# Kernel optimization log

Hardware: AMD Instinct MI355X
Metric: run time of the kernel (lower is better)

## Reference

```python
import jax, jax.numpy as jnp
import numpy as np

N_QUBITS = 8
C64 = jnp.complex64

# ---- gate matrices ----

def u3(t, p, l):
    c = jnp.cos(t / 2).astype(C64)
    s = jnp.sin(t / 2).astype(C64)
    ep = jnp.exp(1j * p).astype(C64)
    el = jnp.exp(1j * l).astype(C64)
    return jnp.stack([jnp.stack([c, -el * s]),
                      jnp.stack([ep * s, ep * el * c])])

def ry(t):
    c = jnp.cos(t / 2).astype(C64)
    s = jnp.sin(t / 2).astype(C64)
    return jnp.stack([jnp.stack([c, -s]), jnp.stack([s, c])])

def rz(t):
    e = jnp.exp(-0.5j * t).astype(C64)
    z = jnp.zeros((), C64)
    return jnp.stack([jnp.stack([e, z]), jnp.stack([z, jnp.conj(e)])])

CNOT = jnp.array([[1, 0, 0, 0], [0, 1, 0, 0], [0, 0, 0, 1], [0, 0, 1, 0]], C64)
PX = jnp.array([[0, 1], [1, 0]], C64)
PY = jnp.array([[0, -1j], [1j, 0]], C64)
PZ = jnp.array([[1, 0], [0, -1]], C64)

# ---- batched state-vector gate application; psi: [B] + [2]*8, wire 0 = axis 1 (MSB) ----

def apply_1q(psi, U, w):
    psi = jnp.moveaxis(psi, w + 1, -1)
    psi = psi @ U.T
    return jnp.moveaxis(psi, -1, w + 1)

def apply_2q(psi, U4, w0, w1):
    psi = jnp.moveaxis(psi, (w0 + 1, w1 + 1), (-2, -1))
    sh = psi.shape
    psi = (psi.reshape(sh[:-2] + (4,)) @ U4.T).reshape(sh)
    return jnp.moveaxis(psi, (-2, -1), (w0 + 1, w1 + 1))

def u_su4(psi, p, w0, w1):
    psi = apply_1q(psi, u3(p[0], p[1], p[2]), w0)
    psi = apply_1q(psi, u3(p[3], p[4], p[5]), w1)
    psi = apply_2q(psi, CNOT, w0, w1)
    psi = apply_1q(psi, ry(p[6]), w0)
    psi = apply_1q(psi, rz(p[7]), w1)
    psi = apply_2q(psi, CNOT, w1, w0)
    psi = apply_1q(psi, ry(p[8]), w0)
    psi = apply_2q(psi, CNOT, w0, w1)
    psi = apply_1q(psi, u3(p[9], p[10], p[11]), w0)
    psi = apply_1q(psi, u3(p[12], p[13], p[14]), w1)
    return psi

LAYER1 = [(0, 1), (2, 3), (4, 5), (6, 7), (1, 2), (3, 4), (5, 6), (7, 0)]
LAYER2 = [(2, 4), (6, 0), (0, 2), (4, 6)]
LAYER3 = [(2, 6)]

def expval(psi, ops):
    phi = psi
    for M, w in ops:
        phi = apply_1q(phi, M, w)
    return jnp.real(jnp.sum(jnp.conj(psi) * phi, axis=tuple(range(1, N_QUBITS + 1))))

def circuit(x, weights):
    # amplitude embedding with normalization
    psi = (x / jnp.linalg.norm(x, axis=1, keepdims=True)).astype(C64)
    psi = psi.reshape((x.shape[0],) + (2,) * N_QUBITS)
    npc = 15
    layers = [LAYER1, LAYER1, LAYER2, LAYER2, LAYER3]
    for i, wires in enumerate(layers):
        p = weights[i * npc:(i + 1) * npc]
        for (w0, w1) in wires:
            psi = u_su4(psi, p, w0, w1)
    meas = [
        expval(psi, [(PX, 2)]), expval(psi, [(PY, 2)]), expval(psi, [(PZ, 2)]),
        expval(psi, [(PX, 6)]), expval(psi, [(PY, 6)]), expval(psi, [(PZ, 6)]),
        expval(psi, [(PX, 2), (PX, 6)]),
        expval(psi, [(PY, 2), (PY, 6)]),
        expval(psi, [(PZ, 2), (PZ, 6)]),
    ]
    return jnp.stack(meas, axis=1)  # [B, 9]


def setup_inputs() -> dict:
    key = jax.random.key(0)
    k1, k2 = jax.random.split(key)
    x = jax.random.normal(k1, (8192, 256), dtype=jnp.float32)
    weights = jax.random.normal(k2, (75,), dtype=jnp.float32)
    return {"x": x, "weights": weights}


def reference(x, weights):
    return circuit(x, weights)
```

## Files before the change

### kernel.cpp

```cpp
#include <hip/hip_runtime.h>

typedef float f32x2 __attribute__((ext_vector_type(2)));
typedef f32x2 c32;

__device__ __forceinline__ c32 mkc(float x, float y) { c32 r; r[0] = x; r[1] = y; return r; }

__device__ __forceinline__ c32 cmul(c32 a, c32 b) {
    c32 r;
    asm("v_pk_mul_f32 %0, %1, %2 op_sel:[0,0] op_sel_hi:[0,1]\n\t"
        "v_pk_fma_f32 %0, %1, %2, %0 op_sel:[1,1,0] op_sel_hi:[1,0,1] neg_lo:[1,0,0]"
        : "=&v"(r) : "v"(a), "v"(b));
    return r;
}
__device__ __forceinline__ c32 cmad(c32 a, c32 b, c32 acc) {
    asm("v_pk_fma_f32 %0, %1, %2, %0 op_sel:[0,0,0] op_sel_hi:[0,1,1]\n\t"
        "v_pk_fma_f32 %0, %1, %2, %0 op_sel:[1,1,0] op_sel_hi:[1,0,1] neg_lo:[1,0,0]"
        : "+v"(acc) : "v"(a), "v"(b));
    return acc;
}


__device__ __forceinline__ void mk_u3(float th, float ph, float la, c32 U[2][2]) {
    float ct = cosf(0.5f * th), st = sinf(0.5f * th);
    U[0][0] = mkc(ct, 0.f);
    U[0][1] = mkc(-cosf(la) * st, -sinf(la) * st);
    U[1][0] = mkc(cosf(ph) * st, sinf(ph) * st);
    U[1][1] = mkc(cosf(ph + la) * ct, sinf(ph + la) * ct);
}

__device__ __forceinline__ void lmul_kron(const c32 A[2][2], const c32 B[2][2], c32 m[4]) {
    c32 t[4];
#pragma unroll
    for (int r = 0; r < 4; ++r) {
        c32 acc = mkc(0.f, 0.f);
#pragma unroll
        for (int k = 0; k < 4; ++k)
            acc = cmad(cmul(A[r >> 1][k >> 1], B[r & 1][k & 1]), m[k], acc);
        t[r] = acc;
    }
#pragma unroll
    for (int r = 0; r < 4; ++r) m[r] = t[r];
}

__device__ void build_col(const float* __restrict__ w, int t, c32* gml) {
    const int g = t >> 2, c = t & 3;
    const float* p = w + g * 15;
    const int c0 = c >> 1, c1 = c & 1;
    c32 A[2][2], B[2][2], m[4], tmp;

    mk_u3(p[0], p[1], p[2], A);
    mk_u3(p[3], p[4], p[5], B);
#pragma unroll
    for (int r = 0; r < 4; ++r) m[r] = cmul(A[r >> 1][c0], B[r & 1][c1]);
    tmp = m[2]; m[2] = m[3]; m[3] = tmp;
    {
        float cc = cosf(0.5f * p[6]), s = sinf(0.5f * p[6]);
        A[0][0] = mkc(cc, 0.f); A[0][1] = mkc(-s, 0.f);
        A[1][0] = mkc(s, 0.f);  A[1][1] = mkc(cc, 0.f);
        float cz = cosf(0.5f * p[7]), sz = sinf(0.5f * p[7]);
        B[0][0] = mkc(cz, -sz); B[0][1] = mkc(0.f, 0.f);
        B[1][0] = mkc(0.f, 0.f); B[1][1] = mkc(cz, sz);
        lmul_kron(A, B, m);
    }
    tmp = m[1]; m[1] = m[3]; m[3] = tmp;
    {
        float cc = cosf(0.5f * p[8]), s = sinf(0.5f * p[8]);
        A[0][0] = mkc(cc, 0.f); A[0][1] = mkc(-s, 0.f);
        A[1][0] = mkc(s, 0.f);  A[1][1] = mkc(cc, 0.f);
        B[0][0] = mkc(1.f, 0.f); B[0][1] = mkc(0.f, 0.f);
        B[1][0] = mkc(0.f, 0.f); B[1][1] = mkc(1.f, 0.f);
        lmul_kron(A, B, m);
    }
    tmp = m[2]; m[2] = m[3]; m[3] = tmp;
    mk_u3(p[9], p[10], p[11], A);
    mk_u3(p[12], p[13], p[14], B);
    lmul_kron(A, B, m);
#pragma unroll
    for (int r = 0; r < 4; ++r) gml[g * 16 + r * 4 + c] = m[r];
}


#define STRIDE 260

__device__ __forceinline__ int swz8(int i) { return i ^ (i >> 4); }
__host__ __device__ constexpr int cswz8(int i) { return i ^ (i >> 4); }

template<int P3, int P2, int P1, int P0>
struct BitMap {
    __device__ static int scatterDyn(int v) {
        return (((v >> 3) & 1) << P3) | (((v >> 2) & 1) << P2) |
               (((v >> 1) & 1) << P1) | ((v & 1) << P0);
    }
    static constexpr int scatter(int v) {
        return (((v >> 3) & 1) << P3) | (((v >> 2) & 1) << P2) |
               (((v >> 1) & 1) << P1) | ((v & 1) << P0);
    }
};

using WA = BitMap<7, 6, 5, 4>;  using LA = BitMap<3, 2, 1, 0>;
using WB = BitMap<3, 2, 1, 0>;  using LB = BitMap<7, 6, 5, 4>;
using WC = BitMap<7, 4, 3, 0>;  using LC = BitMap<6, 5, 2, 1>;
using WD = BitMap<7, 5, 3, 1>;  using LD = BitMap<6, 4, 2, 0>;

template<class WO, class LO, class WN, class LN>
__device__ __forceinline__ void transition(c32* sl, int c, c32 s[16]) {
    const int uo = swz8(LO::scatterDyn(c));
#pragma unroll
    for (int r = 0; r < 16; ++r) sl[uo ^ cswz8(WO::scatter(r))] = s[r];
    const int un = swz8(LN::scatterDyn(c));
#pragma unroll
    for (int r = 0; r < 16; ++r) s[r] = sl[un ^ cswz8(WN::scatter(r))];
}

constexpr int freePos(int A, int B, int k) {
    int cnt = 0;
    for (int p = 0; p < 4; ++p)
        if (p != A && p != B) { if (cnt == k) return p; ++cnt; }
    return -1;
}

template<int A, int B>
__device__ __forceinline__ void gate(const c32 m[16], c32 s[16]) {
    constexpr int C0 = freePos(A, B, 0);
    constexpr int C1 = freePos(A, B, 1);
#pragma unroll
    for (int q = 0; q < 4; ++q) {
        const int base = ((q & 1) << C0) | (((q >> 1) & 1) << C1);
        const int i00 = base, i01 = base | (1 << B), i10 = base | (1 << A),
                  i11 = base | (1 << A) | (1 << B);
        c32 a0 = s[i00], a1 = s[i01], a2 = s[i10], a3 = s[i11];
        c32 r0 = cmul(m[0],  a0); r0 = cmad(m[1],  a1, r0); r0 = cmad(m[2],  a2, r0); r0 = cmad(m[3],  a3, r0);
        c32 r1 = cmul(m[4],  a0); r1 = cmad(m[5],  a1, r1); r1 = cmad(m[6],  a2, r1); r1 = cmad(m[7],  a3, r1);
        c32 r2 = cmul(m[8],  a0); r2 = cmad(m[9],  a1, r2); r2 = cmad(m[10], a2, r2); r2 = cmad(m[11], a3, r2);
        c32 r3 = cmul(m[12], a0); r3 = cmad(m[13], a1, r3); r3 = cmad(m[14], a2, r3); r3 = cmad(m[15], a3, r3);
        s[i00] = r0; s[i01] = r1; s[i10] = r2; s[i11] = r3;
    }
}

__device__ __forceinline__ void loadm(const c32* gml, int idx, c32 m[16]) {
#pragma unroll
    for (int k = 0; k < 16; ++k) m[k] = gml[idx * 16 + k];
}

__global__ __launch_bounds__(64, 4) void sim_kernel(const float* __restrict__ x,
                                                    const float* __restrict__ w,
                                                    float* __restrict__ out) {
    __shared__ c32 TR[4 * STRIDE];
    __shared__ c32 GML[80];
    const int lane = threadIdx.x;
    const int st   = lane >> 4;
    const int c    = lane & 15;
    const int b    = blockIdx.x * 4 + st;

    const float* xb = x + (size_t)b * 256 + c;
    float v[16];
#pragma unroll
    for (int r = 0; r < 16; ++r) v[r] = xb[r << 4];

    if (lane < 20) build_col(w, lane, GML);

    float ss = 0.f;
#pragma unroll
    for (int r = 0; r < 16; ++r) ss = fmaf(v[r], v[r], ss);
#pragma unroll
    for (int o = 8; o; o >>= 1) ss += __shfl_xor(ss, o, 64);
    const float inv = 1.0f / sqrtf(ss);
    c32 s[16];
#pragma unroll
    for (int r = 0; r < 16; ++r) s[r] = mkc(v[r] * inv, 0.f);

    c32* sl = TR + st * STRIDE;
    c32 m[16];

#pragma unroll 1
    for (int pass = 0; pass < 2; ++pass) {
        loadm(GML, pass, m);
        gate<3, 2>(m, s); gate<1, 0>(m, s); gate<2, 1>(m, s);
        transition<WA, LA, WB, LB>(sl, c, s);
        gate<3, 2>(m, s); gate<1, 0>(m, s); gate<2, 1>(m, s);
        transition<WB, LB, WC, LC>(sl, c, s);
        gate<2, 1>(m, s); gate<0, 3>(m, s);
        if (pass == 0) transition<WC, LC, WA, LA>(sl, c, s);
        else           transition<WC, LC, WD, LD>(sl, c, s);
    }

#pragma unroll 1
    for (int pp = 0; pp < 2; ++pp) {
        loadm(GML, 2 + pp, m);
        gate<2, 1>(m, s); gate<0, 3>(m, s);
        gate<3, 2>(m, s); gate<1, 0>(m, s);
    }
    loadm(GML, 4, m);
    gate<2, 0>(m, s);

    float e0 = 0, e1 = 0, e2 = 0, e3 = 0, e4 = 0, e5 = 0, e6 = 0, e7 = 0, e8 = 0;
#pragma unroll
    for (int q = 0; q < 4; ++q) {
        const int f = ((q & 1) << 1) | ((q & 2) << 2);
        c32 a00 = s[f], a01 = s[f | 1], a10 = s[f | 4], a11 = s[f | 5];
        float n00 = a00[0] * a00[0] + a00[1] * a00[1];
        float n01 = a01[0] * a01[0] + a01[1] * a01[1];
        float n10 = a10[0] * a10[0] + a10[1] * a10[1];
        float n11 = a11[0] * a11[0] + a11[1] * a11[1];
        float z2r = a00[0] * a10[0] + a00[1] * a10[1] + a01[0] * a11[0] + a01[1] * a11[1];
        float z2i = a00[0] * a10[1] - a00[1] * a10[0] + a01[0] * a11[1] - a01[1] * a11[0];
        float z6r = a00[0] * a01[0] + a00[1] * a01[1] + a10[0] * a11[0] + a10[1] * a11[1];
        float z6i = a00[0] * a01[1] - a00[1] * a01[0] + a10[0] * a11[1] - a10[1] * a11[0];
        float w1r = a00[0] * a11[0] + a00[1] * a11[1];
        float w2r = a01[0] * a10[0] + a01[1] * a10[1];
        e0 += 2.f * z2r;  e1 += 2.f * z2i;  e2 += n00 + n01 - n10 - n11;
        e3 += 2.f * z6r;  e4 += 2.f * z6i;  e5 += n00 - n01 + n10 - n11;
        e6 += 2.f * (w1r + w2r);  e7 += 2.f * (w2r - w1r);
        e8 += n00 - n01 - n10 + n11;
    }
    float e[9] = {e0, e1, e2, e3, e4, e5, e6, e7, e8};
#pragma unroll
    for (int mm = 0; mm < 9; ++mm) {
        float vv = e[mm];
#pragma unroll
        for (int o = 8; o; o >>= 1) vv += __shfl_xor(vv, o, 64);
        e[mm] = vv;
    }
    if (c == 0) {
#pragma unroll
        for (int mm = 0; mm < 9; ++mm) out[b * 9 + mm] = e[mm];
    }
}

extern "C" void kernel_launch(void* const* d_in, const int* in_sizes, int n_in,
                              void* d_out, int out_size, void* d_ws, size_t ws_size,
                              hipStream_t stream) {
    const float* x = (const float*)d_in[0];
    const float* w = (const float*)d_in[1];
    float* out = (float*)d_out;

    const int batch = in_sizes[0] / 256;
    const int nblocks = batch / 4;
    hipLaunchKernelGGL(sim_kernel, dim3(nblocks), dim3(64), 0, stream, x, w, out);
}
```

Measured before the change: 29.24 us.

## Process two state vectors per thread group and use fast trig intrinsics

Each wavefront now simulates eight samples instead of four: every 16-lane group holds two interleaved state vectors. Gates, LDS transposes and epilogues run on both, so each loaded gate matrix is reused across two states and there is more independent work per thread for latency hiding. The grid is halved and launch bounds are relaxed to one wave per EU, which raises register pressure and lowers occupancy. Gate-matrix construction also switches to the fast __sinf/__cosf intrinsics, which are less accurate.

```diff
diff --git a/kernel.cpp b/kernel.cpp
--- a/kernel.cpp
+++ b/kernel.cpp
@@ -21,11 +21,11 @@
 
 
 __device__ __forceinline__ void mk_u3(float th, float ph, float la, c32 U[2][2]) {
-    float ct = cosf(0.5f * th), st = sinf(0.5f * th);
+    float ct = __cosf(0.5f * th), st = __sinf(0.5f * th);
     U[0][0] = mkc(ct, 0.f);
-    U[0][1] = mkc(-cosf(la) * st, -sinf(la) * st);
-    U[1][0] = mkc(cosf(ph) * st, sinf(ph) * st);
-    U[1][1] = mkc(cosf(ph + la) * ct, sinf(ph + la) * ct);
+    U[0][1] = mkc(-__cosf(la) * st, -__sinf(la) * st);
+    U[1][0] = mkc(__cosf(ph) * st, __sinf(ph) * st);
+    U[1][1] = mkc(__cosf(ph + la) * ct, __sinf(ph + la) * ct);
 }
 
 __device__ __forceinline__ void lmul_kron(const c32 A[2][2], const c32 B[2][2], c32 m[4]) {
@@ -35,7 +35,7 @@
         c32 acc = mkc(0.f, 0.f);
 #pragma unroll
         for (int k = 0; k < 4; ++k)
-            acc = cmad(cmul(A[r >> 1][k >> 1], B[r & 1][k & 1]), m[k], acc);
+            acc = cmad(cmul(A[r >> 1][k >> 1], B[r & 1][k >> 0 & 1]), m[k], acc);
         t[r] = acc;
     }
 #pragma unroll
@@ -54,17 +54,17 @@
     for (int r = 0; r < 4; ++r) m[r] = cmul(A[r >> 1][c0], B[r & 1][c1]);
     tmp = m[2]; m[2] = m[3]; m[3] = tmp;
     {
-        float cc = cosf(0.5f * p[6]), s = sinf(0.5f * p[6]);
+        float cc = __cosf(0.5f * p[6]), s = __sinf(0.5f * p[6]);
         A[0][0] = mkc(cc, 0.f); A[0][1] = mkc(-s, 0.f);
         A[1][0] = mkc(s, 0.f);  A[1][1] = mkc(cc, 0.f);
-        float cz = cosf(0.5f * p[7]), sz = sinf(0.5f * p[7]);
+        float cz = __cosf(0.5f * p[7]), sz = __sinf(0.5f * p[7]);
         B[0][0] = mkc(cz, -sz); B[0][1] = mkc(0.f, 0.f);
         B[1][0] = mkc(0.f, 0.f); B[1][1] = mkc(cz, sz);
         lmul_kron(A, B, m);
     }
     tmp = m[1]; m[1] = m[3]; m[3] = tmp;
     {
-        float cc = cosf(0.5f * p[8]), s = sinf(0.5f * p[8]);
+        float cc = __cosf(0.5f * p[8]), s = __sinf(0.5f * p[8]);
         A[0][0] = mkc(cc, 0.f); A[0][1] = mkc(-s, 0.f);
         A[1][0] = mkc(s, 0.f);  A[1][1] = mkc(cc, 0.f);
         B[0][0] = mkc(1.f, 0.f); B[0][1] = mkc(0.f, 0.f);
@@ -103,13 +103,18 @@
 using WD = BitMap<7, 5, 3, 1>;  using LD = BitMap<6, 4, 2, 0>;
 
 template<class WO, class LO, class WN, class LN>
-__device__ __forceinline__ void transition(c32* sl, int c, c32 s[16]) {
+__device__ __forceinline__ void transition2(c32* slA, c32* slB, int c,
+                                            c32 sA[16], c32 sB[16]) {
     const int uo = swz8(LO::scatterDyn(c));
 #pragma unroll
-    for (int r = 0; r < 16; ++r) sl[uo ^ cswz8(WO::scatter(r))] = s[r];
+    for (int r = 0; r < 16; ++r) slA[uo ^ cswz8(WO::scatter(r))] = sA[r];
+#pragma unroll
+    for (int r = 0; r < 16; ++r) slB[uo ^ cswz8(WO::scatter(r))] = sB[r];
     const int un = swz8(LN::scatterDyn(c));
 #pragma unroll
-    for (int r = 0; r < 16; ++r) s[r] = sl[un ^ cswz8(WN::scatter(r))];
+    for (int r = 0; r < 16; ++r) sA[r] = slA[un ^ cswz8(WN::scatter(r))];
+#pragma unroll
+    for (int r = 0; r < 16; ++r) sB[r] = slB[un ^ cswz8(WN::scatter(r))];
 }
 
 constexpr int freePos(int A, int B, int k) {
@@ -137,62 +142,19 @@
     }
 }
 
+template<int A, int B>
+__device__ __forceinline__ void gate2(const c32 m[16], c32 sA[16], c32 sB[16]) {
+    gate<A, B>(m, sA);
+    gate<A, B>(m, sB);
+}
+
 __device__ __forceinline__ void loadm(const c32* gml, int idx, c32 m[16]) {
 #pragma unroll
     for (int k = 0; k < 16; ++k) m[k] = gml[idx * 16 + k];
 }
 
-__global__ __launch_bounds__(64, 4) void sim_kernel(const float* __restrict__ x,
-                                                    const float* __restrict__ w,
-                                                    float* __restrict__ out) {
-    __shared__ c32 TR[4 * STRIDE];
-    __shared__ c32 GML[80];
-    const int lane = threadIdx.x;
-    const int st   = lane >> 4;
-    const int c    = lane & 15;
-    const int b    = blockIdx.x * 4 + st;
-
-    const float* xb = x + (size_t)b * 256 + c;
-    float v[16];
-#pragma unroll
-    for (int r = 0; r < 16; ++r) v[r] = xb[r << 4];
-
-    if (lane < 20) build_col(w, lane, GML);
-
-    float ss = 0.f;
-#pragma unroll
-    for (int r = 0; r < 16; ++r) ss = fmaf(v[r], v[r], ss);
-#pragma unroll
-    for (int o = 8; o; o >>= 1) ss += __shfl_xor(ss, o, 64);
-    const float inv = 1.0f / sqrtf(ss);
-    c32 s[16];
-#pragma unroll
-    for (int r = 0; r < 16; ++r) s[r] = mkc(v[r] * inv, 0.f);
-
-    c32* sl = TR + st * STRIDE;
-    c32 m[16];
-
-#pragma unroll 1
-    for (int pass = 0; pass < 2; ++pass) {
-        loadm(GML, pass, m);
-        gate<3, 2>(m, s); gate<1, 0>(m, s); gate<2, 1>(m, s);
-        transition<WA, LA, WB, LB>(sl, c, s);
-        gate<3, 2>(m, s); gate<1, 0>(m, s); gate<2, 1>(m, s);
-        transition<WB, LB, WC, LC>(sl, c, s);
-        gate<2, 1>(m, s); gate<0, 3>(m, s);
-        if (pass == 0) transition<WC, LC, WA, LA>(sl, c, s);
-        else           transition<WC, LC, WD, LD>(sl, c, s);
-    }
-
-#pragma unroll 1
-    for (int pp = 0; pp < 2; ++pp) {
-        loadm(GML, 2 + pp, m);
-        gate<2, 1>(m, s); gate<0, 3>(m, s);
-        gate<3, 2>(m, s); gate<1, 0>(m, s);
-    }
-    loadm(GML, 4, m);
-    gate<2, 0>(m, s);
-
+__device__ __forceinline__ void epilogue(const c32 s[16], int c, int b,
+                                         float* __restrict__ out) {
     float e0 = 0, e1 = 0, e2 = 0, e3 = 0, e4 = 0, e5 = 0, e6 = 0, e7 = 0, e8 = 0;
 #pragma unroll
     for (int q = 0; q < 4; ++q) {
@@ -227,6 +189,67 @@
     }
 }
 
+__global__ __launch_bounds__(64, 1) void sim_kernel(const float* __restrict__ x,
+                                                    const float* __restrict__ w,
+                                                    float* __restrict__ out) {
+    __shared__ c32 TR[8 * STRIDE];
+    __shared__ c32 GML[80];
+    const int lane = threadIdx.x;
+    const int st   = lane >> 4;
+    const int c    = lane & 15;
+    const int bA   = blockIdx.x * 8 + st;
+    const int bB   = bA + 4;
+
+    const float* xbA = x + (size_t)bA * 256 + c;
+    const float* xbB = x + (size_t)bB * 256 + c;
+    float vA[16], vB[16];
+#pragma unroll
+    for (int r = 0; r < 16; ++r) vA[r] = xbA[r << 4];
+#pragma unroll
+    for (int r = 0; r < 16; ++r) vB[r] = xbB[r << 4];
+
+    if (lane < 20) build_col(w, lane, GML);
+
+    float ssA = 0.f, ssB = 0.f;
+#pragma unroll
+    for (int r = 0; r < 16; ++r) { ssA = fmaf(vA[r], vA[r], ssA); ssB = fmaf(vB[r], vB[r], ssB); }
+#pragma unroll
+    for (int o = 8; o; o >>= 1) { ssA += __shfl_xor(ssA, o, 64); ssB += __shfl_xor(ssB, o, 64); }
+    const float invA = 1.0f / sqrtf(ssA);
+    const float invB = 1.0f / sqrtf(ssB);
+    c32 sA[16], sB[16];
+#pragma unroll
+    for (int r = 0; r < 16; ++r) { sA[r] = mkc(vA[r] * invA, 0.f); sB[r] = mkc(vB[r] * invB, 0.f); }
+
+    c32* slA = TR + st * STRIDE;
+    c32* slB = TR + (st + 4) * STRIDE;
+    c32 m[16];
+
+#pragma unroll 1
+    for (int pass = 0; pass < 2; ++pass) {
+        loadm(GML, pass, m);
+        gate2<3, 2>(m, sA, sB); gate2<1, 0>(m, sA, sB); gate2<2, 1>(m, sA, sB);
+        transition2<WA, LA, WB, LB>(slA, slB, c, sA, sB);
+        gate2<3, 2>(m, sA, sB); gate2<1, 0>(m, sA, sB); gate2<2, 1>(m, sA, sB);
+        transition2<WB, LB, WC, LC>(slA, slB, c, sA, sB);
+        gate2<2, 1>(m, sA, sB); gate2<0, 3>(m, sA, sB);
+        if (pass == 0) transition2<WC, LC, WA, LA>(slA, slB, c, sA, sB);
+        else           transition2<WC, LC, WD, LD>(slA, slB, c, sA, sB);
+    }
+
+#pragma unroll 1
+    for (int pp = 0; pp < 2; ++pp) {
+        loadm(GML, 2 + pp, m);
+        gate2<2, 1>(m, sA, sB); gate2<0, 3>(m, sA, sB);
+        gate2<3, 2>(m, sA, sB); gate2<1, 0>(m, sA, sB);
+    }
+    loadm(GML, 4, m);
+    gate2<2, 0>(m, sA, sB);
+
+    epilogue(sA, c, bA, out);
+    epilogue(sB, c, bB, out);
+}
+
 extern "C" void kernel_launch(void* const* d_in, const int* in_sizes, int n_in,
                               void* d_out, int out_size, void* d_ws, size_t ws_size,
                               hipStream_t stream) {
@@ -235,6 +258,6 @@
     float* out = (float*)d_out;
 
     const int batch = in_sizes[0] / 256;
-    const int nblocks = batch / 4;
+    const int nblocks = batch / 8;
     hipLaunchKernelGGL(sim_kernel, dim3(nblocks), dim3(64), 0, stream, x, w, out);
 }
```

Result: faster. 27.11 us (-7.3%).
